# Kernel optimization log

Measured on AMD Instinct MI355X. Metric: run time of the kernel, lower is better.

The kernel has to match this reference:

```python
import jax, jax.numpy as jnp
import numpy as np

COMMITMENT_COST = 0.25
NUM_EMBEDDINGS = 512
EMBEDDING_DIM = 64


def setup_inputs() -> dict:
    key = jax.random.key(0)
    k1, k2 = jax.random.split(key)
    inputs = jax.random.normal(k1, (64, EMBEDDING_DIM, 32, 32), dtype=jnp.float32)
    # nn.Embedding init: uniform(-1/K, 1/K)
    emb_w = jax.random.uniform(
        k2, (NUM_EMBEDDINGS, EMBEDDING_DIM), dtype=jnp.float32,
        minval=-1.0 / NUM_EMBEDDINGS, maxval=1.0 / NUM_EMBEDDINGS)
    return {"inputs": inputs, "emb_w": emb_w}


def reference(inputs, emb_w):
    sg = jax.lax.stop_gradient
    # NCHW -> NHWC
    x = jnp.transpose(inputs, (0, 2, 3, 1))          # [B, H, W, D]
    B, H, W, D = x.shape
    flat = x.reshape(-1, D)                          # [N, D]
    dist = (jnp.sum(flat * flat, axis=1, keepdims=True)
            + jnp.sum(emb_w * emb_w, axis=1)
            - 2.0 * jnp.dot(flat, emb_w.T))          # [N, K]
    idx = jnp.argmin(dist, axis=1)                   # [N]
    # one-hot @ emb_w is just a gather
    quantized = emb_w[idx].reshape(B, H, W, D)       # [B, H, W, D]
    e_latent_loss = jnp.mean((sg(quantized) - x) ** 2)
    q_latent_loss = jnp.mean((quantized - sg(x)) ** 2)
    loss = q_latent_loss + COMMITMENT_COST * e_latent_loss
    # straight-through estimator
    quantized_st = x + sg(quantized - x)
    out = jnp.transpose(quantized_st, (0, 3, 1, 2))  # back to NCHW
    return loss, out, idx[:, None]
```

## Files before the change

kernel.cpp:

```cpp
#include <hip/hip_runtime.h>


#define D_     64
#define HW_    1024
#define N_     65536
#define K_     512
#define M_     128
#define NDTOT  (N_ * D_)
#define XP     160
#define EP     256

__global__ __launch_bounds__(256, 1) void vq_fused_kernel(const float* __restrict__ inp,
                                                          const float* __restrict__ emb,
                                                          float* __restrict__ out) {
    __shared__ float ldsx[D_ * XP];
    __shared__ float ldse[D_ * EP];
    __shared__ float ldsn[K_];
    __shared__ float sxs[M_];
    __shared__ int   fi[M_];
    __shared__ float psum[256];

    const int tid  = threadIdx.x;
    const int lane = tid & 63;
    const int w    = tid >> 6;
    const int pg   = lane & 7;
    const int kg   = lane >> 3;
    const int n0   = blockIdx.x * M_;
    const int b    = n0 >> 10;
    const int hw0  = n0 & 1023;
    const float* xbase = inp + b * (D_ * HW_) + hw0;

#pragma unroll
    for (int i = 0; i < 8; ++i) {
        int q = i * 256 + tid;
        int d = q >> 5;
        int pq = q & 31;
        float4 v = *(const float4*)(xbase + d * HW_ + pq * 4);
        *(float4*)(ldsx + d * XP + (pq >> 2) * 20 + (pq & 3) * 4) = v;
    }
#pragma unroll
    for (int c = 0; c < 2; ++c) {
        const int k = c * 256 + tid;
        const float* e = emb + k * D_;
        float el[64];
#pragma unroll
        for (int q = 0; q < 16; ++q) {
            float4 v = *(const float4*)(e + q * 4);
            el[4 * q + 0] = v.x; el[4 * q + 1] = v.y;
            el[4 * q + 2] = v.z; el[4 * q + 3] = v.w;
        }
        float r[8];
#pragma unroll
        for (int j = 0; j < 8; ++j) r[j] = __fmul_rn(el[j], el[j]);
#pragma unroll
        for (int i = 1; i < 8; ++i)
#pragma unroll
            for (int j = 0; j < 8; ++j)
                r[j] = __fadd_rn(r[j], __fmul_rn(el[i * 8 + j], el[i * 8 + j]));
        ldsn[k] = __fadd_rn(__fadd_rn(__fadd_rn(r[0], r[1]), __fadd_rn(r[2], r[3])),
                            __fadd_rn(__fadd_rn(r[4], r[5]), __fadd_rn(r[6], r[7])));
    }
#pragma unroll
    for (int i = 0; i < 16; ++i) {
        float4 v = *(const float4*)(emb + tid * D_ + i * 4);
        ldse[(i * 4 + 0) * EP + tid] = v.x;
        ldse[(i * 4 + 1) * EP + tid] = v.y;
        ldse[(i * 4 + 2) * EP + tid] = v.z;
        ldse[(i * 4 + 3) * EP + tid] = v.w;
    }
    __syncthreads();

    if (tid < M_) {
        const int xb2 = (tid >> 4) * 20 + (tid & 15);
        float r[8];
#pragma unroll
        for (int j = 0; j < 8; ++j) {
            float v = ldsx[j * XP + xb2];
            r[j] = __fmul_rn(v, v);
        }
#pragma unroll
        for (int i = 1; i < 8; ++i)
#pragma unroll
            for (int j = 0; j < 8; ++j) {
                float v = ldsx[(i * 8 + j) * XP + xb2];
                r[j] = __fadd_rn(r[j], __fmul_rn(v, v));
            }
        sxs[tid] = __fadd_rn(__fadd_rn(__fadd_rn(r[0], r[1]), __fadd_rn(r[2], r[3])),
                             __fadd_rn(__fadd_rn(r[4], r[5]), __fadd_rn(r[6], r[7])));
    }
    __syncthreads();

    float sxp[16];
    {
        float4 s0 = *(const float4*)(sxs + pg * 16);
        float4 s1 = *(const float4*)(sxs + pg * 16 + 4);
        float4 s2 = *(const float4*)(sxs + pg * 16 + 8);
        float4 s3 = *(const float4*)(sxs + pg * 16 + 12);
        sxp[0]=s0.x; sxp[1]=s0.y; sxp[2]=s0.z; sxp[3]=s0.w;
        sxp[4]=s1.x; sxp[5]=s1.y; sxp[6]=s1.z; sxp[7]=s1.w;
        sxp[8]=s2.x; sxp[9]=s2.y; sxp[10]=s2.z; sxp[11]=s2.w;
        sxp[12]=s3.x; sxp[13]=s3.y; sxp[14]=s3.z; sxp[15]=s3.w;
    }
    float runv[16];
    int   runi[16];
#pragma unroll
    for (int j = 0; j < 16; ++j) { runv[j] = 3.4e38f; runi[j] = 0; }

#pragma unroll 1
    for (int c = 0; c < 2; ++c) {
        if (c) {
            __syncthreads();
#pragma unroll
            for (int i = 0; i < 16; ++i) {
                float4 v = *(const float4*)(emb + (256 + tid) * D_ + i * 4);
                ldse[(i * 4 + 0) * EP + tid] = v.x;
                ldse[(i * 4 + 1) * EP + tid] = v.y;
                ldse[(i * 4 + 2) * EP + tid] = v.z;
                ldse[(i * 4 + 3) * EP + tid] = v.w;
            }
            __syncthreads();
        }
        float nk[8];
        {
            float4 na = *(const float4*)(ldsn + c * 256 + w * 64 + kg * 8);
            float4 nb = *(const float4*)(ldsn + c * 256 + w * 64 + kg * 8 + 4);
            nk[0]=na.x; nk[1]=na.y; nk[2]=na.z; nk[3]=na.w;
            nk[4]=nb.x; nk[5]=nb.y; nk[6]=nb.z; nk[7]=nb.w;
        }
        float acc[16][8];
#pragma unroll
        for (int j = 0; j < 16; ++j)
#pragma unroll
            for (int q = 0; q < 8; ++q) acc[j][q] = 0.f;

        const float* xcol = ldsx + pg * 20;
        const float* ecol = ldse + (w << 6) + (kg << 3);
#pragma unroll 4
        for (int d = 0; d < 64; ++d) {
            const float* xr = xcol + d * XP;
            float4 xa = *(const float4*)(xr);
            float4 xb4 = *(const float4*)(xr + 4);
            float4 xc4 = *(const float4*)(xr + 8);
            float4 xd4 = *(const float4*)(xr + 12);
            const float* er = ecol + d * EP;
            float4 ea = *(const float4*)(er);
            float4 eb = *(const float4*)(er + 4);
            float xv[16] = {xa.x, xa.y, xa.z, xa.w, xb4.x, xb4.y, xb4.z, xb4.w,
                            xc4.x, xc4.y, xc4.z, xc4.w, xd4.x, xd4.y, xd4.z, xd4.w};
            float ev[8]  = {ea.x, ea.y, ea.z, ea.w, eb.x, eb.y, eb.z, eb.w};
#pragma unroll
            for (int j = 0; j < 16; ++j)
#pragma unroll
                for (int q = 0; q < 8; ++q)
                    acc[j][q] = fmaf(xv[j], ev[q], acc[j][q]);
        }

        const int kidx0 = c * 256 + w * 64 + kg * 8;
#pragma unroll
        for (int j = 0; j < 16; ++j) {
            float sx = sxp[j];
#pragma unroll
            for (int q = 0; q < 8; ++q) {
                float t = __fadd_rn(sx, nk[q]);
                float v = __fadd_rn(t, -2.0f * acc[j][q]);
                if (v < runv[j]) { runv[j] = v; runi[j] = kidx0 + q; }
            }
        }
    }

    __syncthreads();
    float* mv = ldse;
    int*   mi = (int*)(ldse + 128 * 33);
    const int col = w * 8 + kg;
#pragma unroll
    for (int j = 0; j < 16; ++j) {
        int p = pg * 16 + j;
        mv[p * 33 + col] = runv[j];
        mi[p * 33 + col] = runi[j];
    }
    __syncthreads();
    if (tid < M_) {
        float bv = 3.4e38f; int bi = 0x7fffffff;
#pragma unroll
        for (int g = 0; g < 32; ++g) {
            float v  = mv[tid * 33 + g];
            int   ii = mi[tid * 33 + g];
            if (v < bv || (v == bv && ii < bi)) { bv = v; bi = ii; }
        }
        fi[tid] = bi;
        out[1 + NDTOT + n0 + tid] = (float)bi;
    }
    __syncthreads();

    {
        const int p  = tid & 127;
        const int dh = tid >> 7;
        const float* er2 = emb + fi[p] * D_ + dh * 32;
        float ev2[32];
#pragma unroll
        for (int q = 0; q < 8; ++q) {
            float4 v = *(const float4*)(er2 + 4 * q);
            ev2[4 * q + 0] = v.x; ev2[4 * q + 1] = v.y;
            ev2[4 * q + 2] = v.z; ev2[4 * q + 3] = v.w;
        }
        float* ob = out + 1 + b * (D_ * HW_) + hw0 + p;
        const int xb2 = (p >> 4) * 20 + (p & 15);
        float local = 0.f;
#pragma unroll
        for (int dd = 0; dd < 32; ++dd) {
            float xv = ldsx[(dh * 32 + dd) * XP + xb2];
            float df = ev2[dd] - xv;
            local = fmaf(df, df, local);
            ob[(dh * 32 + dd) * HW_] = ev2[dd];
        }
        psum[tid] = local;
    }
    __syncthreads();
    if (tid < 64) {
        float s = psum[tid] + psum[tid + 64] + psum[tid + 128] + psum[tid + 192];
#pragma unroll
        for (int off = 32; off > 0; off >>= 1)
            s += __shfl_down(s, off, 64);
        if (tid == 0)
            atomicAdd(out, s * (1.25f / (float)NDTOT));
    }
}

extern "C" void kernel_launch(void* const* d_in, const int* in_sizes, int n_in,
                              void* d_out, int out_size, void* d_ws, size_t ws_size,
                              hipStream_t stream) {
    const float* inp = (const float*)d_in[0];
    const float* emb = (const float*)d_in[1];
    float* out = (float*)d_out;
    (void)d_ws; (void)ws_size;

    hipMemsetAsync(d_out, 0, sizeof(float), stream);
    vq_fused_kernel<<<512, 256, 0, stream>>>(inp, emb, out);
}
```

Baseline: 153.5 us.

## Double block tile to 256 points with 512 threads, reuse codebook tile

Each block now handles 256 spatial points with 512 threads and 256 blocks in total. Each thread still computes a 16x8 tile, but threads are now mapped to 16 point groups by 32 code groups, so each staged codebook half in LDS serves twice as many points. This halves how often the codebook is reloaded and norms recomputed per point, and launch bounds now ask for 2 blocks per CU. The cost is more LDS per block, only 256 blocks for 256 CUs (one wave of work), and a distance step changed to use an FMA, which may alter rounding in ties.

```diff
diff --git a/kernel.cpp b/kernel.cpp
--- a/kernel.cpp
+++ b/kernel.cpp
@@ -5,43 +5,39 @@
 #define HW_    1024
 #define N_     65536
 #define K_     512
-#define M_     128
+#define M_     256
+#define XPITCH 288
+#define EPITCH 256
 #define NDTOT  (N_ * D_)
-#define XP     160
-#define EP     256
-
-__global__ __launch_bounds__(256, 1) void vq_fused_kernel(const float* __restrict__ inp,
+
+__global__ __launch_bounds__(512, 2) void vq_fused_kernel(const float* __restrict__ inp,
                                                           const float* __restrict__ emb,
                                                           float* __restrict__ out) {
-    __shared__ float ldsx[D_ * XP];
-    __shared__ float ldse[D_ * EP];
+    __shared__ float ldsx[D_ * XPITCH];
+    __shared__ float ldse[16896];
     __shared__ float ldsn[K_];
     __shared__ float sxs[M_];
     __shared__ int   fi[M_];
-    __shared__ float psum[256];
-
-    const int tid  = threadIdx.x;
-    const int lane = tid & 63;
-    const int w    = tid >> 6;
-    const int pg   = lane & 7;
-    const int kg   = lane >> 3;
-    const int n0   = blockIdx.x * M_;
-    const int b    = n0 >> 10;
-    const int hw0  = n0 & 1023;
+    __shared__ float psum[512];
+
+    const int tid = threadIdx.x;
+    const int pg  = tid & 15;
+    const int kg  = tid >> 4;
+    const int n0  = blockIdx.x * M_;
+    const int b   = n0 >> 10;
+    const int hw0 = n0 & 1023;
     const float* xbase = inp + b * (D_ * HW_) + hw0;
 
 #pragma unroll
     for (int i = 0; i < 8; ++i) {
-        int q = i * 256 + tid;
-        int d = q >> 5;
-        int pq = q & 31;
-        float4 v = *(const float4*)(xbase + d * HW_ + pq * 4);
-        *(float4*)(ldsx + d * XP + (pq >> 2) * 20 + (pq & 3) * 4) = v;
-    }
-#pragma unroll
-    for (int c = 0; c < 2; ++c) {
-        const int k = c * 256 + tid;
-        const float* e = emb + k * D_;
+        int q = i * 512 + tid;
+        int d = q >> 6;
+        int s = q & 63;
+        float4 v = *(const float4*)(xbase + d * HW_ + s * 4);
+        *(float4*)(ldsx + d * XPITCH + (s >> 3) * 36 + (s & 7) * 4) = v;
+    }
+    {
+        const float* e = emb + tid * D_;
         float el[64];
 #pragma unroll
         for (int q = 0; q < 16; ++q) {
@@ -57,32 +53,37 @@
 #pragma unroll
             for (int j = 0; j < 8; ++j)
                 r[j] = __fadd_rn(r[j], __fmul_rn(el[i * 8 + j], el[i * 8 + j]));
-        ldsn[k] = __fadd_rn(__fadd_rn(__fadd_rn(r[0], r[1]), __fadd_rn(r[2], r[3])),
-                            __fadd_rn(__fadd_rn(r[4], r[5]), __fadd_rn(r[6], r[7])));
-    }
-#pragma unroll
-    for (int i = 0; i < 16; ++i) {
-        float4 v = *(const float4*)(emb + tid * D_ + i * 4);
-        ldse[(i * 4 + 0) * EP + tid] = v.x;
-        ldse[(i * 4 + 1) * EP + tid] = v.y;
-        ldse[(i * 4 + 2) * EP + tid] = v.z;
-        ldse[(i * 4 + 3) * EP + tid] = v.w;
+        ldsn[tid] = __fadd_rn(__fadd_rn(__fadd_rn(r[0], r[1]), __fadd_rn(r[2], r[3])),
+                              __fadd_rn(__fadd_rn(r[4], r[5]), __fadd_rn(r[6], r[7])));
+    }
+    {
+        const int k  = tid & 255;
+        const int dh = (tid >> 8) * 32;
+        const float* er = emb + k * D_ + dh;
+#pragma unroll
+        for (int j = 0; j < 8; ++j) {
+            float4 v = *(const float4*)(er + j * 4);
+            ldse[(dh + j * 4 + 0) * EPITCH + k] = v.x;
+            ldse[(dh + j * 4 + 1) * EPITCH + k] = v.y;
+            ldse[(dh + j * 4 + 2) * EPITCH + k] = v.z;
+            ldse[(dh + j * 4 + 3) * EPITCH + k] = v.w;
+        }
     }
     __syncthreads();
 
     if (tid < M_) {
-        const int xb2 = (tid >> 4) * 20 + (tid & 15);
+        const int colb = (tid >> 5) * 36 + (tid & 31);
         float r[8];
 #pragma unroll
         for (int j = 0; j < 8; ++j) {
-            float v = ldsx[j * XP + xb2];
+            float v = ldsx[j * XPITCH + colb];
             r[j] = __fmul_rn(v, v);
         }
 #pragma unroll
         for (int i = 1; i < 8; ++i)
 #pragma unroll
             for (int j = 0; j < 8; ++j) {
-                float v = ldsx[(i * 8 + j) * XP + xb2];
+                float v = ldsx[(i * 8 + j) * XPITCH + colb];
                 r[j] = __fadd_rn(r[j], __fmul_rn(v, v));
             }
         sxs[tid] = __fadd_rn(__fadd_rn(__fadd_rn(r[0], r[1]), __fadd_rn(r[2], r[3])),
@@ -90,79 +91,73 @@
     }
     __syncthreads();
 
-    float sxp[16];
-    {
-        float4 s0 = *(const float4*)(sxs + pg * 16);
-        float4 s1 = *(const float4*)(sxs + pg * 16 + 4);
-        float4 s2 = *(const float4*)(sxs + pg * 16 + 8);
-        float4 s3 = *(const float4*)(sxs + pg * 16 + 12);
-        sxp[0]=s0.x; sxp[1]=s0.y; sxp[2]=s0.z; sxp[3]=s0.w;
-        sxp[4]=s1.x; sxp[5]=s1.y; sxp[6]=s1.z; sxp[7]=s1.w;
-        sxp[8]=s2.x; sxp[9]=s2.y; sxp[10]=s2.z; sxp[11]=s2.w;
-        sxp[12]=s3.x; sxp[13]=s3.y; sxp[14]=s3.z; sxp[15]=s3.w;
-    }
     float runv[16];
     int   runi[16];
 #pragma unroll
     for (int j = 0; j < 16; ++j) { runv[j] = 3.4e38f; runi[j] = 0; }
+
+    const float* xcol = ldsx + (pg >> 1) * 36 + (pg & 1) * 16;
+    const float* ecol = ldse + kg * 8;
 
 #pragma unroll 1
     for (int c = 0; c < 2; ++c) {
         if (c) {
             __syncthreads();
-#pragma unroll
-            for (int i = 0; i < 16; ++i) {
-                float4 v = *(const float4*)(emb + (256 + tid) * D_ + i * 4);
-                ldse[(i * 4 + 0) * EP + tid] = v.x;
-                ldse[(i * 4 + 1) * EP + tid] = v.y;
-                ldse[(i * 4 + 2) * EP + tid] = v.z;
-                ldse[(i * 4 + 3) * EP + tid] = v.w;
+            const int k  = tid & 255;
+            const int dh = (tid >> 8) * 32;
+            const float* er = emb + (256 + k) * D_ + dh;
+#pragma unroll
+            for (int j = 0; j < 8; ++j) {
+                float4 v = *(const float4*)(er + j * 4);
+                ldse[(dh + j * 4 + 0) * EPITCH + k] = v.x;
+                ldse[(dh + j * 4 + 1) * EPITCH + k] = v.y;
+                ldse[(dh + j * 4 + 2) * EPITCH + k] = v.z;
+                ldse[(dh + j * 4 + 3) * EPITCH + k] = v.w;
             }
             __syncthreads();
         }
+
+        float acc[16][8];
+#pragma unroll
+        for (int j = 0; j < 16; ++j)
+#pragma unroll
+            for (int q = 0; q < 8; ++q) acc[j][q] = 0.f;
+
+#pragma unroll 2
+        for (int d = 0; d < 64; ++d) {
+            const float* xr = xcol + d * XPITCH;
+            float4 xa = *(const float4*)(xr);
+            float4 xb = *(const float4*)(xr + 4);
+            float4 xc = *(const float4*)(xr + 8);
+            float4 xd = *(const float4*)(xr + 12);
+            const float* er = ecol + d * EPITCH;
+            float4 ea = *(const float4*)(er);
+            float4 eb = *(const float4*)(er + 4);
+            float xv[16] = {xa.x, xa.y, xa.z, xa.w, xb.x, xb.y, xb.z, xb.w,
+                            xc.x, xc.y, xc.z, xc.w, xd.x, xd.y, xd.z, xd.w};
+            float ev[8]  = {ea.x, ea.y, ea.z, ea.w, eb.x, eb.y, eb.z, eb.w};
+#pragma unroll
+            for (int j = 0; j < 16; ++j)
+#pragma unroll
+                for (int q = 0; q < 8; ++q)
+                    acc[j][q] = fmaf(xv[j], ev[q], acc[j][q]);
+        }
+
+        const int kidx0 = c * 256 + kg * 8;
         float nk[8];
         {
-            float4 na = *(const float4*)(ldsn + c * 256 + w * 64 + kg * 8);
-            float4 nb = *(const float4*)(ldsn + c * 256 + w * 64 + kg * 8 + 4);
+            float4 na = *(const float4*)(ldsn + kidx0);
+            float4 nb = *(const float4*)(ldsn + kidx0 + 4);
             nk[0]=na.x; nk[1]=na.y; nk[2]=na.z; nk[3]=na.w;
             nk[4]=nb.x; nk[5]=nb.y; nk[6]=nb.z; nk[7]=nb.w;
         }
-        float acc[16][8];
-#pragma unroll
-        for (int j = 0; j < 16; ++j)
-#pragma unroll
-            for (int q = 0; q < 8; ++q) acc[j][q] = 0.f;
-
-        const float* xcol = ldsx + pg * 20;
-        const float* ecol = ldse + (w << 6) + (kg << 3);
-#pragma unroll 4
-        for (int d = 0; d < 64; ++d) {
-            const float* xr = xcol + d * XP;
-            float4 xa = *(const float4*)(xr);
-            float4 xb4 = *(const float4*)(xr + 4);
-            float4 xc4 = *(const float4*)(xr + 8);
-            float4 xd4 = *(const float4*)(xr + 12);
-            const float* er = ecol + d * EP;
-            float4 ea = *(const float4*)(er);
-            float4 eb = *(const float4*)(er + 4);
-            float xv[16] = {xa.x, xa.y, xa.z, xa.w, xb4.x, xb4.y, xb4.z, xb4.w,
-                            xc4.x, xc4.y, xc4.z, xc4.w, xd4.x, xd4.y, xd4.z, xd4.w};
-            float ev[8]  = {ea.x, ea.y, ea.z, ea.w, eb.x, eb.y, eb.z, eb.w};
-#pragma unroll
-            for (int j = 0; j < 16; ++j)
-#pragma unroll
-                for (int q = 0; q < 8; ++q)
-                    acc[j][q] = fmaf(xv[j], ev[q], acc[j][q]);
-        }
-
-        const int kidx0 = c * 256 + w * 64 + kg * 8;
 #pragma unroll
         for (int j = 0; j < 16; ++j) {
-            float sx = sxp[j];
+            const float sx = sxs[pg * 16 + j];
 #pragma unroll
             for (int q = 0; q < 8; ++q) {
                 float t = __fadd_rn(sx, nk[q]);
-                float v = __fadd_rn(t, -2.0f * acc[j][q]);
+                float v = fmaf(-2.0f, acc[j][q], t);
                 if (v < runv[j]) { runv[j] = v; runi[j] = kidx0 + q; }
             }
         }
@@ -170,13 +165,12 @@
 
     __syncthreads();
     float* mv = ldse;
-    int*   mi = (int*)(ldse + 128 * 33);
-    const int col = w * 8 + kg;
+    int*   mi = (int*)(ldse + 256 * 33);
 #pragma unroll
     for (int j = 0; j < 16; ++j) {
         int p = pg * 16 + j;
-        mv[p * 33 + col] = runv[j];
-        mi[p * 33 + col] = runi[j];
+        mv[p * 33 + kg] = runv[j];
+        mi[p * 33 + kg] = runi[j];
     }
     __syncthreads();
     if (tid < M_) {
@@ -193,9 +187,9 @@
     __syncthreads();
 
     {
-        const int p  = tid & 127;
-        const int dh = tid >> 7;
-        const float* er2 = emb + fi[p] * D_ + dh * 32;
+        const int p  = tid & 255;
+        const int dh = (tid >> 8) * 32;
+        const float* er2 = emb + fi[p] * D_ + dh;
         float ev2[32];
 #pragma unroll
         for (int q = 0; q < 8; ++q) {
@@ -204,20 +198,22 @@
             ev2[4 * q + 2] = v.z; ev2[4 * q + 3] = v.w;
         }
         float* ob = out + 1 + b * (D_ * HW_) + hw0 + p;
-        const int xb2 = (p >> 4) * 20 + (p & 15);
+        const int colb = (p >> 5) * 36 + (p & 31);
         float local = 0.f;
 #pragma unroll
         for (int dd = 0; dd < 32; ++dd) {
-            float xv = ldsx[(dh * 32 + dd) * XP + xb2];
+            float xv = ldsx[(dh + dd) * XPITCH + colb];
             float df = ev2[dd] - xv;
             local = fmaf(df, df, local);
-            ob[(dh * 32 + dd) * HW_] = ev2[dd];
+            ob[(dh + dd) * HW_] = ev2[dd];
         }
         psum[tid] = local;
     }
     __syncthreads();
     if (tid < 64) {
-        float s = psum[tid] + psum[tid + 64] + psum[tid + 128] + psum[tid + 192];
+        float s = 0.f;
+#pragma unroll
+        for (int g = 0; g < 8; ++g) s += psum[tid + 64 * g];
 #pragma unroll
         for (int off = 32; off > 0; off >>= 1)
             s += __shfl_down(s, off, 64);
@@ -235,5 +231,5 @@
     (void)d_ws; (void)ws_size;
 
     hipMemsetAsync(d_out, 0, sizeof(float), stream);
-    vq_fused_kernel<<<512, 256, 0, stream>>>(inp, emb, out);
+    vq_fused_kernel<<<256, 512, 0, stream>>>(inp, emb, out);
 }
```

Measured after the change: 132.2 us. -13.9%, faster.
